# Optimization experiments

Measured on AMD Instinct MI355X. Metric: run time of the kernel, lower is better.

The kernel has to match this reference:

```python
import jax, jax.numpy as jnp
import numpy as np

B, S, D = 4, 16, 512          # batch, seq, attention_dim
V, T = 32000, 18              # vocab_size, tree_depth
INNER = V - 1                 # internal nodes of Huffman tree


def setup_inputs() -> dict:
    key = jax.random.key(0)
    k_att, k_w, k_idx, k_bit = jax.random.split(key, 4)
    att = jax.random.normal(k_att, (B, S, D), dtype=jnp.float32)
    weight = jax.random.normal(k_w, (INNER, D), dtype=jnp.float32) * 0.02
    path_index = jax.random.randint(k_idx, (V * T,), 0, INNER, dtype=jnp.int64)
    # left/right branch bits: sign=+1,bias=0 -> p ; sign=-1,bias=1 -> 1-p
    bits = jax.random.randint(k_bit, (V * T,), 0, 2).astype(jnp.float32)
    path_sign = 1.0 - 2.0 * bits
    path_bias = bits
    return {
        "att": att,
        "weight": weight,
        "path_index": path_index,
        "path_sign": path_sign,
        "path_bias": path_bias,
        "vocab_size": V,
        "tree_depth": T,
    }


def reference(att, weight, path_index, path_sign, path_bias, vocab_size, tree_depth):
    # h: sigmoid of linear projection onto internal-node vectors  [B,S,INNER]
    h = jax.nn.sigmoid(jnp.einsum("bsd,nd->bsn", att, weight))
    # gather per-(token,depth) internal-node probs, flip via sign/bias
    g = jnp.take(h, path_index, axis=-1) * path_sign + path_bias  # [B,S,V*T]
    Hm = g.reshape(att.shape[0], -1, vocab_size, tree_depth)      # [B,S,V,T]
    return jnp.sum(jnp.log(Hm), axis=-1)                          # [B,S,V]
```

## Files before the change

### kernel.cpp

```cpp
#include <hip/hip_runtime.h>
#include <hip/hip_bf16.h>

#define BS    64
#define DDIM  512
#define NV    32000
#define TD    18
#define INNER 31999
#define NPAD  32000

typedef __attribute__((ext_vector_type(8))) short short8;
typedef __attribute__((ext_vector_type(4))) float floatx4;

__device__ __forceinline__ float bf16_to_f32(unsigned short u) {
    union { unsigned int i; float f; } v; v.i = ((unsigned int)u) << 16; return v.f;
}
__device__ __forceinline__ unsigned short f32_to_bf16(float f) {
    union { float f; unsigned int i; } v; v.f = f;
    unsigned int r = v.i + 0x7FFFu + ((v.i >> 16) & 1u);
    return (unsigned short)(r >> 16);
}

#define IDXB 2250
__global__ __launch_bounds__(256) void prep(
    const int* __restrict__ idx,
    const unsigned int* __restrict__ signbits,
    unsigned short* __restrict__ idx2,
    const float4* __restrict__ att,
    ushort4* __restrict__ attb)
{
    const int b = blockIdx.x;
    if (b < IDXB) {
        const unsigned int* w = (const unsigned int*)idx;
        bool i64 = true;
#pragma unroll
        for (int j = 1; j < 16; j += 2) i64 &= (w[j] == 0u);
        int i = b * 256 + threadIdx.x;
        int val = i64 ? idx[2 * i] : idx[i];
        idx2[i] = (unsigned short)((val << 1) | (int)(signbits[i] >> 31));
    } else {
        int i = (b - IDXB) * 256 + threadIdx.x;
        float4 a = att[i];
        ushort4 r;
        r.x = f32_to_bf16(a.x); r.y = f32_to_bf16(a.y);
        r.z = f32_to_bf16(a.z); r.w = f32_to_bf16(a.w);
        attb[i] = r;
    }
}

__global__ __launch_bounds__(256) void gemm_logsig(
    const unsigned short* __restrict__ attb,
    const float* __restrict__ weight,
    unsigned int* __restrict__ pairsT)
{
    const int lane = threadIdx.x & 63;
    const int wave = threadIdx.x >> 6;
    const int nb   = blockIdx.x * 64 + wave * 16;
    const int l15  = lane & 15;
    const int quad = lane >> 4;

    floatx4 acc[4];
#pragma unroll
    for (int i = 0; i < 4; ++i) acc[i] = (floatx4){0.f, 0.f, 0.f, 0.f};

    int brow = nb + l15;
    if (brow > INNER - 1) brow = INNER - 1;
    const float*          bbase = weight + (size_t)brow * DDIM + quad * 8;
    const unsigned short* abase = attb + l15 * DDIM + quad * 8;

#pragma unroll 4
    for (int k0 = 0; k0 < DDIM; k0 += 32) {
        float4 b0 = *(const float4*)(bbase + k0);
        float4 b1 = *(const float4*)(bbase + k0 + 4);
        short8 bfrag;
        bfrag[0] = (short)f32_to_bf16(b0.x); bfrag[1] = (short)f32_to_bf16(b0.y);
        bfrag[2] = (short)f32_to_bf16(b0.z); bfrag[3] = (short)f32_to_bf16(b0.w);
        bfrag[4] = (short)f32_to_bf16(b1.x); bfrag[5] = (short)f32_to_bf16(b1.y);
        bfrag[6] = (short)f32_to_bf16(b1.z); bfrag[7] = (short)f32_to_bf16(b1.w);
#pragma unroll
        for (int mt = 0; mt < 4; ++mt) {
            short8 afrag = *(const short8*)(abase + mt * 16 * DDIM + k0);
            acc[mt] = __builtin_amdgcn_mfma_f32_16x16x32_bf16(afrag, bfrag, acc[mt], 0, 0, 0);
        }
    }

    const int n = nb + l15;
    if (n < INNER) {
        unsigned int* dst = pairsT + (size_t)n * 64 + quad * 4;
#pragma unroll
        for (int mt = 0; mt < 4; ++mt) {
            uint4 pk;
#pragma unroll
            for (int r = 0; r < 4; ++r) {
                float x = acc[mt][r];
                float lp = -(fmaxf(-x, 0.f) + __logf(1.f + __expf(-fabsf(x))));
                float lm = lp - x;
                ((unsigned int*)&pk)[r] = (unsigned int)f32_to_bf16(lp)
                                        | ((unsigned int)f32_to_bf16(lm) << 16);
            }
            *(uint4*)(dst + mt * 16) = pk;
        }
    }
}

__global__ __launch_bounds__(256) void gather_T(
    const unsigned int* __restrict__ pairsT,
    const unsigned short* __restrict__ idx2,
    float* __restrict__ out)
{
    const int lane = threadIdx.x & 63;
    const int wave = threadIdx.x >> 6;

#pragma unroll
    for (int g = 0; g < 4; ++g) {
        const int v0 = blockIdx.x * 64 + wave * 16 + g * 4;
        const unsigned short* ip = idx2 + (size_t)v0 * TD;
        float a0 = 0.f, a1 = 0.f, a2 = 0.f, a3 = 0.f;
#pragma unroll
        for (int t = 0; t < TD; ++t) {
            unsigned int e0 = __builtin_amdgcn_readfirstlane(ip[t]);
            unsigned int e1 = __builtin_amdgcn_readfirstlane(ip[TD + t]);
            unsigned int e2 = __builtin_amdgcn_readfirstlane(ip[2 * TD + t]);
            unsigned int e3 = __builtin_amdgcn_readfirstlane(ip[3 * TD + t]);
            unsigned int p0 = pairsT[(size_t)(e0 >> 1) * 64 + lane];
            unsigned int p1 = pairsT[(size_t)(e1 >> 1) * 64 + lane];
            unsigned int p2 = pairsT[(size_t)(e2 >> 1) * 64 + lane];
            unsigned int p3 = pairsT[(size_t)(e3 >> 1) * 64 + lane];
            a0 += bf16_to_f32((e0 & 1u) ? (unsigned short)(p0 >> 16) : (unsigned short)(p0 & 0xFFFFu));
            a1 += bf16_to_f32((e1 & 1u) ? (unsigned short)(p1 >> 16) : (unsigned short)(p1 & 0xFFFFu));
            a2 += bf16_to_f32((e2 & 1u) ? (unsigned short)(p2 >> 16) : (unsigned short)(p2 & 0xFFFFu));
            a3 += bf16_to_f32((e3 & 1u) ? (unsigned short)(p3 >> 16) : (unsigned short)(p3 & 0xFFFFu));
        }
        float4 st = {a0, a1, a2, a3};
        *(float4*)(out + (size_t)lane * NV + v0) = st;
    }
}

extern "C" void kernel_launch(void* const* d_in, const int* in_sizes, int n_in,
                              void* d_out, int out_size, void* d_ws, size_t ws_size,
                              hipStream_t stream)
{
    const float4*       att4   = (const float4*)d_in[0];
    const float*        weight = (const float*)d_in[1];
    const int*          pidx   = (const int*)d_in[2];
    const unsigned int* psign  = (const unsigned int*)d_in[3];
    float* out = (float*)d_out;

    char* ws = (char*)d_ws;
    unsigned int*   pairsT = (unsigned int*)ws;
    unsigned short* idx2   = (unsigned short*)(ws + 8192000);
    unsigned short* attb   = (unsigned short*)(ws + 9344000);

    prep<<<IDXB + 32, 256, 0, stream>>>(pidx, psign, idx2, att4, (ushort4*)attb);
    gemm_logsig<<<500, 256, 0, stream>>>(attb, weight, pairsT);
    gather_T<<<500, 256, 0, stream>>>(pairsT, idx2, out);
}
```

Before: 145.2 us.

## Remove prep kernel; convert att in GEMM and decode indices in gather

Drops the separate prep kernel. The GEMM now loads fp32 activations and converts them to bf16 inline, and the gather kernel reads the raw int64/int32 path indices and sign bits directly instead of a packed 16-bit index array. This removes one launch and the write-then-read of the intermediate idx2 and attb buffers. In exchange, the gather reads wider index data (8-byte indices plus 4-byte signs) and each GEMM block redoes the activation conversion.

```diff
diff --git a/kernel.cpp b/kernel.cpp
--- a/kernel.cpp
+++ b/kernel.cpp
@@ -19,36 +19,19 @@
     unsigned int r = v.i + 0x7FFFu + ((v.i >> 16) & 1u);
     return (unsigned short)(r >> 16);
 }
-
-#define IDXB 2250
-__global__ __launch_bounds__(256) void prep(
-    const int* __restrict__ idx,
-    const unsigned int* __restrict__ signbits,
-    unsigned short* __restrict__ idx2,
-    const float4* __restrict__ att,
-    ushort4* __restrict__ attb)
-{
-    const int b = blockIdx.x;
-    if (b < IDXB) {
-        const unsigned int* w = (const unsigned int*)idx;
-        bool i64 = true;
-#pragma unroll
-        for (int j = 1; j < 16; j += 2) i64 &= (w[j] == 0u);
-        int i = b * 256 + threadIdx.x;
-        int val = i64 ? idx[2 * i] : idx[i];
-        idx2[i] = (unsigned short)((val << 1) | (int)(signbits[i] >> 31));
-    } else {
-        int i = (b - IDXB) * 256 + threadIdx.x;
-        float4 a = att[i];
-        ushort4 r;
-        r.x = f32_to_bf16(a.x); r.y = f32_to_bf16(a.y);
-        r.z = f32_to_bf16(a.z); r.w = f32_to_bf16(a.w);
-        attb[i] = r;
-    }
+__device__ __forceinline__ short8 cvt8(const float* p) {
+    float4 a = *(const float4*)p;
+    float4 b = *(const float4*)(p + 4);
+    short8 f;
+    f[0] = (short)f32_to_bf16(a.x); f[1] = (short)f32_to_bf16(a.y);
+    f[2] = (short)f32_to_bf16(a.z); f[3] = (short)f32_to_bf16(a.w);
+    f[4] = (short)f32_to_bf16(b.x); f[5] = (short)f32_to_bf16(b.y);
+    f[6] = (short)f32_to_bf16(b.z); f[7] = (short)f32_to_bf16(b.w);
+    return f;
 }
 
 __global__ __launch_bounds__(256) void gemm_logsig(
-    const unsigned short* __restrict__ attb,
+    const float* __restrict__ att,
     const float* __restrict__ weight,
     unsigned int* __restrict__ pairsT)
 {
@@ -64,21 +47,15 @@
 
     int brow = nb + l15;
     if (brow > INNER - 1) brow = INNER - 1;
-    const float*          bbase = weight + (size_t)brow * DDIM + quad * 8;
-    const unsigned short* abase = attb + l15 * DDIM + quad * 8;
+    const float* bbase = weight + (size_t)brow * DDIM + quad * 8;
+    const float* abase = att + l15 * DDIM + quad * 8;
 
 #pragma unroll 4
     for (int k0 = 0; k0 < DDIM; k0 += 32) {
-        float4 b0 = *(const float4*)(bbase + k0);
-        float4 b1 = *(const float4*)(bbase + k0 + 4);
-        short8 bfrag;
-        bfrag[0] = (short)f32_to_bf16(b0.x); bfrag[1] = (short)f32_to_bf16(b0.y);
-        bfrag[2] = (short)f32_to_bf16(b0.z); bfrag[3] = (short)f32_to_bf16(b0.w);
-        bfrag[4] = (short)f32_to_bf16(b1.x); bfrag[5] = (short)f32_to_bf16(b1.y);
-        bfrag[6] = (short)f32_to_bf16(b1.z); bfrag[7] = (short)f32_to_bf16(b1.w);
+        short8 bfrag = cvt8(bbase + k0);
 #pragma unroll
         for (int mt = 0; mt < 4; ++mt) {
-            short8 afrag = *(const short8*)(abase + mt * 16 * DDIM + k0);
+            short8 afrag = cvt8(abase + mt * 16 * DDIM + k0);
             acc[mt] = __builtin_amdgcn_mfma_f32_16x16x32_bf16(afrag, bfrag, acc[mt], 0, 0, 0);
         }
     }
@@ -104,31 +81,43 @@
 
 __global__ __launch_bounds__(256) void gather_T(
     const unsigned int* __restrict__ pairsT,
-    const unsigned short* __restrict__ idx2,
+    const int* __restrict__ idx,
+    const unsigned int* __restrict__ signbits,
     float* __restrict__ out)
 {
     const int lane = threadIdx.x & 63;
     const int wave = threadIdx.x >> 6;
 
+    const unsigned int* w = (const unsigned int*)idx;
+    unsigned int orw = 0;
+#pragma unroll
+    for (int j = 1; j < 16; j += 2) orw |= w[j];
+    const bool i64 = (orw == 0u);
+
 #pragma unroll
     for (int g = 0; g < 4; ++g) {
         const int v0 = blockIdx.x * 64 + wave * 16 + g * 4;
-        const unsigned short* ip = idx2 + (size_t)v0 * TD;
+        const int i0 = v0 * TD;
         float a0 = 0.f, a1 = 0.f, a2 = 0.f, a3 = 0.f;
 #pragma unroll
         for (int t = 0; t < TD; ++t) {
-            unsigned int e0 = __builtin_amdgcn_readfirstlane(ip[t]);
-            unsigned int e1 = __builtin_amdgcn_readfirstlane(ip[TD + t]);
-            unsigned int e2 = __builtin_amdgcn_readfirstlane(ip[2 * TD + t]);
-            unsigned int e3 = __builtin_amdgcn_readfirstlane(ip[3 * TD + t]);
-            unsigned int p0 = pairsT[(size_t)(e0 >> 1) * 64 + lane];
-            unsigned int p1 = pairsT[(size_t)(e1 >> 1) * 64 + lane];
-            unsigned int p2 = pairsT[(size_t)(e2 >> 1) * 64 + lane];
-            unsigned int p3 = pairsT[(size_t)(e3 >> 1) * 64 + lane];
-            a0 += bf16_to_f32((e0 & 1u) ? (unsigned short)(p0 >> 16) : (unsigned short)(p0 & 0xFFFFu));
-            a1 += bf16_to_f32((e1 & 1u) ? (unsigned short)(p1 >> 16) : (unsigned short)(p1 & 0xFFFFu));
-            a2 += bf16_to_f32((e2 & 1u) ? (unsigned short)(p2 >> 16) : (unsigned short)(p2 & 0xFFFFu));
-            a3 += bf16_to_f32((e3 & 1u) ? (unsigned short)(p3 >> 16) : (unsigned short)(p3 & 0xFFFFu));
+            int j0 = i0 + t, j1 = i0 + TD + t, j2 = i0 + 2 * TD + t, j3 = i0 + 3 * TD + t;
+            unsigned int n0 = __builtin_amdgcn_readfirstlane(i64 ? idx[2 * j0] : idx[j0]);
+            unsigned int n1 = __builtin_amdgcn_readfirstlane(i64 ? idx[2 * j1] : idx[j1]);
+            unsigned int n2 = __builtin_amdgcn_readfirstlane(i64 ? idx[2 * j2] : idx[j2]);
+            unsigned int n3 = __builtin_amdgcn_readfirstlane(i64 ? idx[2 * j3] : idx[j3]);
+            unsigned int s0 = __builtin_amdgcn_readfirstlane(signbits[j0]) >> 31;
+            unsigned int s1 = __builtin_amdgcn_readfirstlane(signbits[j1]) >> 31;
+            unsigned int s2 = __builtin_amdgcn_readfirstlane(signbits[j2]) >> 31;
+            unsigned int s3 = __builtin_amdgcn_readfirstlane(signbits[j3]) >> 31;
+            unsigned int p0 = pairsT[(size_t)n0 * 64 + lane];
+            unsigned int p1 = pairsT[(size_t)n1 * 64 + lane];
+            unsigned int p2 = pairsT[(size_t)n2 * 64 + lane];
+            unsigned int p3 = pairsT[(size_t)n3 * 64 + lane];
+            a0 += bf16_to_f32(s0 ? (unsigned short)(p0 >> 16) : (unsigned short)(p0 & 0xFFFFu));
+            a1 += bf16_to_f32(s1 ? (unsigned short)(p1 >> 16) : (unsigned short)(p1 & 0xFFFFu));
+            a2 += bf16_to_f32(s2 ? (unsigned short)(p2 >> 16) : (unsigned short)(p2 & 0xFFFFu));
+            a3 += bf16_to_f32(s3 ? (unsigned short)(p3 >> 16) : (unsigned short)(p3 & 0xFFFFu));
         }
         float4 st = {a0, a1, a2, a3};
         *(float4*)(out + (size_t)lane * NV + v0) = st;
@@ -139,18 +128,14 @@
                               void* d_out, int out_size, void* d_ws, size_t ws_size,
                               hipStream_t stream)
 {
-    const float4*       att4   = (const float4*)d_in[0];
+    const float*        att    = (const float*)d_in[0];
     const float*        weight = (const float*)d_in[1];
     const int*          pidx   = (const int*)d_in[2];
     const unsigned int* psign  = (const unsigned int*)d_in[3];
     float* out = (float*)d_out;
 
-    char* ws = (char*)d_ws;
-    unsigned int*   pairsT = (unsigned int*)ws;
-    unsigned short* idx2   = (unsigned short*)(ws + 8192000);
-    unsigned short* attb   = (unsigned short*)(ws + 9344000);
+    unsigned int* pairsT = (unsigned int*)d_ws;
 
-    prep<<<IDXB + 32, 256, 0, stream>>>(pidx, psign, idx2, att4, (ushort4*)attb);
-    gemm_logsig<<<500, 256, 0, stream>>>(attb, weight, pairsT);
-    gather_T<<<500, 256, 0, stream>>>(pairsT, idx2, out);
+    gemm_logsig<<<500, 256, 0, stream>>>(att, weight, pairsT);
+    gather_T<<<500, 256, 0, stream>>>(pairsT, pidx, psign, out);
 }
```

After: 164.9 us. 1.14x slower.
